# Performance work log

Hardware: AMD Instinct MI355X
Metric: run time of the kernel (lower is better)

The kernel has to match this reference:

```python
import jax, jax.numpy as jnp
import numpy as np

GAMMA = 2.0
IGNORE_INDEX = 255
REMAP_FROM, REMAP_TO = 255, 0


def setup_inputs() -> dict:
    key = jax.random.key(0)
    k1, k2 = jax.random.split(key)
    B, C, H, W = 8, 21, 512, 512
    inp = jax.random.normal(k1, (B, C, H, W), dtype=jnp.float32)
    target = jax.random.randint(k2, (B, H, W), 0, 21, dtype=jnp.int64)
    return {"input": inp, "target": target}


def reference(input, target):
    B, C = input.shape[0], input.shape[1]
    # [B, C, H, W] -> [B, C, HW] -> [B, HW, C] -> [N, C]
    x = input.reshape(B, C, -1).transpose(0, 2, 1).reshape(-1, C)
    tgt = target.reshape(-1)
    # remap_tensor_digit({255: 0}) applied BEFORE the ignore mask (as in original)
    tgt = jnp.where(tgt == REMAP_FROM, REMAP_TO, tgt)
    logp = jax.nn.log_softmax(x, axis=1)                     # [N, C]
    logpt = jnp.take_along_axis(logp, tgt[:, None], axis=1)[:, 0]  # [N]
    pt = jnp.exp(logpt)
    loss = -((1.0 - pt) ** GAMMA) * logpt
    mask = (tgt != IGNORE_INDEX).astype(loss.dtype)          # all-ones after remap, kept for fidelity
    loss = loss * mask
    return loss.mean()
```

## Files before the change

kernel.cpp:

```cpp
#include <hip/hip_runtime.h>

constexpr int kC     = 21;
constexpr int kHW    = 512 * 512;
constexpr int kB     = 8;
constexpr int kN     = kB * kHW;
constexpr int kQuads = kN / 4;
constexpr int kBlock = 256;
constexpr int kGrid  = kQuads / kBlock;

typedef float fvec4 __attribute__((ext_vector_type(4)));
typedef int   ivec4 __attribute__((ext_vector_type(4)));

__global__ __launch_bounds__(kBlock) void fl_main(const float* __restrict__ x,
                                                  const int* __restrict__ tgt,
                                                  float* __restrict__ part) {
    const int gid = blockIdx.x * kBlock + threadIdx.x;
    const int b   = gid >> 16;
    const int hw4 = gid & 0xFFFF;

    const float* xb = x + (size_t)b * ((size_t)kC * kHW) + (size_t)hw4 * 4;

    ivec4 t4 = __builtin_nontemporal_load(
        reinterpret_cast<const ivec4*>(tgt + (size_t)gid * 4));

    fvec4 v[kC];
#pragma unroll
    for (int c = 0; c < kC; ++c) {
        v[c] = __builtin_nontemporal_load(
            reinterpret_cast<const fvec4*>(xb + (size_t)c * kHW));
    }

    float loss = 0.f;
#pragma unroll
    for (int p = 0; p < 4; ++p) {
        const int t = (t4[p] == 255) ? 0 : t4[p];

        float m = v[0][p];
#pragma unroll
        for (int c = 1; c < kC; ++c) m = fmaxf(m, v[c][p]);

        float s = 0.f, xt = v[0][p];
#pragma unroll
        for (int c = 0; c < kC; ++c) {
            const float xv = v[c][p];
            s += __expf(xv - m);
            if (c == t) xt = xv;
        }

        const float logpt = xt - m - __logf(s);
        const float pt    = __expf(logpt);
        const float om    = 1.f - pt;
        loss += om * om * (-logpt);
    }
    loss *= (1.0f / (float)kN);

#pragma unroll
    for (int off = 32; off > 0; off >>= 1)
        loss += __shfl_down(loss, off, 64);

    __shared__ float ws[kBlock / 64];
    const int lane = threadIdx.x & 63;
    const int wid  = threadIdx.x >> 6;
    if (lane == 0) ws[wid] = loss;
    __syncthreads();
    if (threadIdx.x == 0) {
        part[blockIdx.x] = ws[0] + ws[1] + ws[2] + ws[3];
    }
}

__global__ __launch_bounds__(kBlock) void fl_reduce(const float* __restrict__ part,
                                                    float* __restrict__ out) {
    const int t = threadIdx.x;
    const fvec4 a = *reinterpret_cast<const fvec4*>(part + (size_t)t * 8);
    const fvec4 b = *reinterpret_cast<const fvec4*>(part + (size_t)t * 8 + 4);
    float s = (a[0] + a[1] + a[2] + a[3]) + (b[0] + b[1] + b[2] + b[3]);

#pragma unroll
    for (int off = 32; off > 0; off >>= 1)
        s += __shfl_down(s, off, 64);

    __shared__ float ws[kBlock / 64];
    const int lane = t & 63;
    const int wid  = t >> 6;
    if (lane == 0) ws[wid] = s;
    __syncthreads();
    if (t == 0) out[0] = ws[0] + ws[1] + ws[2] + ws[3];
}

extern "C" void kernel_launch(void* const* d_in, const int* in_sizes, int n_in,
                              void* d_out, int out_size, void* d_ws, size_t ws_size,
                              hipStream_t stream) {
    const float* x   = (const float*)d_in[0];
    const int*   tgt = (const int*)d_in[1];
    float*       out = (float*)d_out;
    float*       part = (float*)d_ws;

    fl_main<<<kGrid, kBlock, 0, stream>>>(x, tgt, part);
    fl_reduce<<<1, kBlock, 0, stream>>>(part, out);
}
```

Before: 230.0 us.

## Stream channels through online softmax with double-buffered loads to cut registers

Replaces holding all 21 channel vectors in registers with an online (running max/sum) softmax over groups of three channels. Loads for the next group are issued before the current group is processed, alternating between two register buffers. It also raises launch bounds to request 8 blocks per CU. The goal is lower VGPR pressure and higher occupancy for this memory-bound kernel, at the cost of extra rescaling exps and fewer loads in flight per thread.

Result: no change. 230.3 us (+0.1%).

```diff
diff --git a/kernel.cpp b/kernel.cpp
--- a/kernel.cpp
+++ b/kernel.cpp
@@ -11,9 +11,9 @@
 typedef float fvec4 __attribute__((ext_vector_type(4)));
 typedef int   ivec4 __attribute__((ext_vector_type(4)));
 
-__global__ __launch_bounds__(kBlock) void fl_main(const float* __restrict__ x,
-                                                  const int* __restrict__ tgt,
-                                                  float* __restrict__ part) {
+__global__ __launch_bounds__(kBlock, 8) void fl_main(const float* __restrict__ x,
+                                                     const int* __restrict__ tgt,
+                                                     float* __restrict__ part) {
     const int gid = blockIdx.x * kBlock + threadIdx.x;
     const int b   = gid >> 16;
     const int hw4 = gid & 0xFFFF;
@@ -22,32 +22,61 @@
 
     ivec4 t4 = __builtin_nontemporal_load(
         reinterpret_cast<const ivec4*>(tgt + (size_t)gid * 4));
+#pragma unroll
+    for (int p = 0; p < 4; ++p) t4[p] = (t4[p] == 255) ? 0 : t4[p];
 
-    fvec4 v[kC];
+    auto LD = [&](int c) -> fvec4 {
+        return __builtin_nontemporal_load(
+            reinterpret_cast<const fvec4*>(xb + (size_t)c * kHW));
+    };
+
+    fvec4 M, S, XT;
+    fvec4 A0, A1, A2, B0, B1, B2;
+
+    A0 = LD(0); A1 = LD(1); A2 = LD(2);
+    B0 = LD(3); B1 = LD(4); B2 = LD(5);
+
 #pragma unroll
-    for (int c = 0; c < kC; ++c) {
-        v[c] = __builtin_nontemporal_load(
-            reinterpret_cast<const fvec4*>(xb + (size_t)c * kHW));
+    for (int p = 0; p < 4; ++p) {
+        const float m = fmaxf(fmaxf(A0[p], A1[p]), A2[p]);
+        M[p] = m;
+        S[p] = __expf(A0[p] - m) + __expf(A1[p] - m) + __expf(A2[p] - m);
+        float xt = A0[p];
+        xt = (t4[p] == 1) ? A1[p] : xt;
+        xt = (t4[p] == 2) ? A2[p] : xt;
+        XT[p] = xt;
     }
+    A0 = LD(6); A1 = LD(7); A2 = LD(8);
+
+#define FL_STEP(V0, V1, V2, CB)                                          \
+    _Pragma("unroll")                                                    \
+    for (int p = 0; p < 4; ++p) {                                        \
+        const float cm = fmaxf(fmaxf(V0[p], V1[p]), V2[p]);              \
+        const float nm = fmaxf(M[p], cm);                                \
+        float s = S[p] * __expf(M[p] - nm);                              \
+        s += __expf(V0[p] - nm);                                         \
+        s += __expf(V1[p] - nm);                                         \
+        s += __expf(V2[p] - nm);                                         \
+        S[p] = s; M[p] = nm;                                             \
+        float xt = XT[p];                                                \
+        xt = (t4[p] == (CB) + 0) ? V0[p] : xt;                           \
+        xt = (t4[p] == (CB) + 1) ? V1[p] : xt;                           \
+        xt = (t4[p] == (CB) + 2) ? V2[p] : xt;                           \
+        XT[p] = xt;                                                      \
+    }
+
+    FL_STEP(B0, B1, B2, 3);   B0 = LD(9);  B1 = LD(10); B2 = LD(11);
+    FL_STEP(A0, A1, A2, 6);   A0 = LD(12); A1 = LD(13); A2 = LD(14);
+    FL_STEP(B0, B1, B2, 9);   B0 = LD(15); B1 = LD(16); B2 = LD(17);
+    FL_STEP(A0, A1, A2, 12);  A0 = LD(18); A1 = LD(19); A2 = LD(20);
+    FL_STEP(B0, B1, B2, 15);
+    FL_STEP(A0, A1, A2, 18);
+#undef FL_STEP
 
     float loss = 0.f;
 #pragma unroll
     for (int p = 0; p < 4; ++p) {
-        const int t = (t4[p] == 255) ? 0 : t4[p];
-
-        float m = v[0][p];
-#pragma unroll
-        for (int c = 1; c < kC; ++c) m = fmaxf(m, v[c][p]);
-
-        float s = 0.f, xt = v[0][p];
-#pragma unroll
-        for (int c = 0; c < kC; ++c) {
-            const float xv = v[c][p];
-            s += __expf(xv - m);
-            if (c == t) xt = xv;
-        }
-
-        const float logpt = xt - m - __logf(s);
+        const float logpt = XT[p] - M[p] - __logf(S[p]);
         const float pt    = __expf(logpt);
         const float om    = 1.f - pt;
         loss += om * om * (-logpt);
@@ -63,9 +92,8 @@
     const int wid  = threadIdx.x >> 6;
     if (lane == 0) ws[wid] = loss;
     __syncthreads();
-    if (threadIdx.x == 0) {
+    if (threadIdx.x == 0)
         part[blockIdx.x] = ws[0] + ws[1] + ws[2] + ws[3];
-    }
 }
 
 __global__ __launch_bounds__(kBlock) void fl_reduce(const float* __restrict__ part,
@@ -90,9 +118,9 @@
 extern "C" void kernel_launch(void* const* d_in, const int* in_sizes, int n_in,
                               void* d_out, int out_size, void* d_ws, size_t ws_size,
                               hipStream_t stream) {
-    const float* x   = (const float*)d_in[0];
-    const int*   tgt = (const int*)d_in[1];
-    float*       out = (float*)d_out;
+    const float* x    = (const float*)d_in[0];
+    const int*   tgt  = (const int*)d_in[1];
+    float*       out  = (float*)d_out;
     float*       part = (float*)d_ws;
 
     fl_main<<<kGrid, kBlock, 0, stream>>>(x, tgt, part);
```
